# Kernel tuning notes

Hardware: AMD Instinct MI355X
Metric: run time of the kernel (lower is better)

## Reference

```python
import jax, jax.numpy as jnp
import numpy as np


def _eta(pos, conj):
    # e[0] = pos[:,1::2] repeated into even/odd cols; e[1] = (+/-)pos[:,0::2] likewise
    c = jnp.repeat(pos[:, 1::2], 2, axis=1)
    s = jnp.repeat(pos[:, 0::2], 2, axis=1)
    return jnp.stack([c, s if conj else -s])  # [2, N, d]


def setup_inputs() -> dict:
    key = jax.random.key(0)
    ks = jax.random.split(key, 8)
    B, N, d, H = 8, 4096, 128, 4
    s = 0.02
    return {
        "x": jax.random.normal(ks[0], (B, N, d), jnp.float32),
        "pos": jax.random.normal(ks[1], (N, d), jnp.float32),
        "W_lt": jax.random.normal(ks[2], (d, d), jnp.float32) * s,
        "W_phi": jax.random.normal(ks[3], (d * H, d), jnp.float32) * s,
        "b_phi": jnp.zeros((d * H,), jnp.float32),
        "W_c1": jax.random.normal(ks[4], (H, H), jnp.float32) * s,
        "b_c1": jnp.zeros((H,), jnp.float32),
        "W_c2": jax.random.normal(ks[5], (1, H), jnp.float32) * s,
        "b_c2": jnp.zeros((1,), jnp.float32),
        "ln_g": jnp.ones((d,), jnp.float32),
        "ln_b": jnp.zeros((d,), jnp.float32),
        "W_f1": jax.random.normal(ks[6], (d, d), jnp.float32) * s,
        "b_f1": jnp.zeros((d,), jnp.float32),
        "W_f2": jax.random.normal(ks[7], (d, d), jnp.float32) * s,
        "b_f2": jnp.zeros((d,), jnp.float32),
    }


def reference(x, pos, W_lt, W_phi, b_phi, W_c1, b_c1, W_c2, b_c2,
              ln_g, ln_b, W_f1, b_f1, W_f2, b_f2):
    B, N, d = x.shape
    H = W_phi.shape[0] // d
    x = x @ W_lt.T                                   # linear_trans (no bias)
    e = _eta(pos, False)                             # [2,N,d]
    xe = x[None] * e[:, None]                        # [2,B,N,d]
    # A = ones(N,N) - I  =>  A @ v == sum over nodes minus self
    f = xe.sum(axis=2, keepdims=True) - xe           # [2,B,N,d]
    f_norm = jnp.sqrt(f[0] ** 2 + f[1] ** 2)         # [B,N,d]
    phi = ((x + pos[None]) @ W_phi.T + b_phi).reshape(B, N, H, d)
    # ReLU1(|f| - phi): relu(min(1, f_norm - phi))
    res = jax.nn.relu(jnp.minimum(1.0, f_norm[:, :, None, :] - phi))  # [B,N,H,d]
    ce = _eta(pos, True)
    fec = f[0] * ce[0][None] - f[1] * ce[1][None]    # [B,N,d]
    rfe = res * fec[:, :, None, :]                   # [B,N,H,d]
    # inverse transform: (1/N) * (M @ A) with A symmetric => sum-minus-self over node dim
    inv = (rfe.sum(axis=1, keepdims=True) - rfe) / N  # [B,N,H,d]
    t = inv.transpose(0, 1, 3, 2)                    # [B,N,d,H]
    comb = (jax.nn.relu(t @ W_c1.T + b_c1) @ W_c2.T + b_c2)[..., 0]  # [B,N,d]
    m = x + comb
    mu = m.mean(-1, keepdims=True)
    var = ((m - mu) ** 2).mean(-1, keepdims=True)
    mn = (m - mu) * jax.lax.rsqrt(var + 1e-6) * ln_g + ln_b
    return jax.nn.relu(mn @ W_f1.T + b_f1) @ W_f2.T + b_f2
```

## Files before the change

kernel.cpp:

```cpp
#include <hip/hip_runtime.h>
#include <hip/hip_bf16.h>


#define DEV __device__ __forceinline__

typedef __attribute__((ext_vector_type(8))) short bf16x8;
typedef __attribute__((ext_vector_type(4))) float f32x4;

constexpr int Bb = 8, Nn = 4096;
constexpr int BN = Bb * Nn;
constexpr int LDP = 136;

union U8 { ushort u[8]; uint4 v; };

static DEV ushort f2bf(float f) {
    __hip_bfloat16 h = __float2bfloat16(f);
    return *reinterpret_cast<ushort*>(&h);
}

template <int MODE>
__global__ __launch_bounds__(256) void k_mfma_gemm(
    const float* __restrict__ X, const float* __restrict__ W,
    const float* __restrict__ bias, const float* __restrict__ pos,
    float* __restrict__ outF, ushort* __restrict__ outB,
    float* __restrict__ PS, float* __restrict__ PT,
    const float* __restrict__ S0c, const float* __restrict__ S1c)
{
    __shared__ __align__(16) ushort xs[64 * LDP];
    __shared__ __align__(16) ushort wsl[128 * LDP];
    __shared__ float red[256];
    const int t = threadIdx.x;
    const int row0 = blockIdx.x * 64;
    const int jt = (MODE == 1) ? blockIdx.y : 0;

    red[t] = 0.f;

    {
        #pragma unroll
        for (int i = 0; i < 4; ++i) {
            int e = t + i * 256, r = e >> 4, c = (e & 15) * 8;
            const float* p = X + (size_t)(row0 + r) * 128 + c;
            float4 a = *reinterpret_cast<const float4*>(p);
            float4 b = *reinterpret_cast<const float4*>(p + 4);
            if (MODE == 1) {
                int n = (row0 + r) & (Nn - 1);
                const float* q = pos + (size_t)n * 128 + c;
                float4 pa = *reinterpret_cast<const float4*>(q);
                float4 pb = *reinterpret_cast<const float4*>(q + 4);
                a.x += pa.x; a.y += pa.y; a.z += pa.z; a.w += pa.w;
                b.x += pb.x; b.y += pb.y; b.z += pb.z; b.w += pb.w;
            }
            U8 u;
            u.u[0] = f2bf(a.x); u.u[1] = f2bf(a.y); u.u[2] = f2bf(a.z); u.u[3] = f2bf(a.w);
            u.u[4] = f2bf(b.x); u.u[5] = f2bf(b.y); u.u[6] = f2bf(b.z); u.u[7] = f2bf(b.w);
            *reinterpret_cast<uint4*>(xs + r * LDP + c) = u.v;
        }
    }
    {
        const float* Wt = W + (size_t)jt * 128 * 128;
        #pragma unroll
        for (int i = 0; i < 8; ++i) {
            int e = t + i * 256, r = e >> 4, c = (e & 15) * 8;
            const float* p = Wt + (size_t)r * 128 + c;
            float4 a = *reinterpret_cast<const float4*>(p);
            float4 b = *reinterpret_cast<const float4*>(p + 4);
            U8 u;
            u.u[0] = f2bf(a.x); u.u[1] = f2bf(a.y); u.u[2] = f2bf(a.z); u.u[3] = f2bf(a.w);
            u.u[4] = f2bf(b.x); u.u[5] = f2bf(b.y); u.u[6] = f2bf(b.z); u.u[7] = f2bf(b.w);
            *reinterpret_cast<uint4*>(wsl + r * LDP + c) = u.v;
        }
    }
    __syncthreads();

    const int w = t >> 6, l = t & 63;
    const int lr = l & 15;
    const int lk = (l >> 4) * 8;

    f32x4 acc[8];
    #pragma unroll
    for (int cf = 0; cf < 8; ++cf) acc[cf] = f32x4{0.f, 0.f, 0.f, 0.f};

    #pragma unroll
    for (int ks = 0; ks < 4; ++ks) {
        bf16x8 a = *reinterpret_cast<const bf16x8*>(xs + (w * 16 + lr) * LDP + ks * 32 + lk);
        #pragma unroll
        for (int cf = 0; cf < 8; ++cf) {
            bf16x8 b = *reinterpret_cast<const bf16x8*>(wsl + (cf * 16 + lr) * LDP + ks * 32 + lk);
            acc[cf] = __builtin_amdgcn_mfma_f32_16x16x32_bf16(a, b, acc[cf], 0, 0, 0);
        }
    }

    const int bidb = row0 >> 12;
    #pragma unroll
    for (int cf = 0; cf < 8; ++cf) {
        int col = cf * 16 + lr;
        if (MODE == 0) {
            float s0c = 0.f, s1c = 0.f;
            #pragma unroll
            for (int reg = 0; reg < 4; ++reg) {
                int r = row0 + w * 16 + (l >> 4) * 4 + reg;
                float o = acc[cf][reg];
                outF[(size_t)r * 128 + col] = o;
                int n = r & (Nn - 1);
                float2 p2 = *reinterpret_cast<const float2*>(pos + (size_t)n * 128 + (col & ~1));
                s0c += o * p2.y;
                s1c += o * p2.x;
            }
            s0c += __shfl_xor(s0c, 16); s0c += __shfl_xor(s0c, 32);
            s1c += __shfl_xor(s1c, 16); s1c += __shfl_xor(s1c, 32);
            if ((l >> 4) == 0) {
                atomicAdd(&red[col], s0c);
                atomicAdd(&red[128 + col], s1c);
            }
        } else {
            float S0v = S0c[bidb * 128 + col];
            float S1v = S1c[bidb * 128 + col];
            float bv = bias[jt * 128 + col];
            float tp = 0.f;
            #pragma unroll
            for (int reg = 0; reg < 4; ++reg) {
                int r = row0 + w * 16 + (l >> 4) * 4 + reg;
                float o = acc[cf][reg] + bv;
                outB[(size_t)r * 512 + jt * 128 + col] = f2bf(o);
                int n = r & (Nn - 1);
                float xv = X[(size_t)r * 128 + col];
                float2 p2 = *reinterpret_cast<const float2*>(pos + (size_t)n * 128 + (col & ~1));
                float cc = p2.y, ss = p2.x;
                float f0 = S0v - xv * cc;
                float f1 = xv * ss - S1v;
                float fn = sqrtf(f0 * f0 + f1 * f1);
                float fec = f0 * cc - f1 * ss;
                float res = fmaxf(0.f, fminf(1.f, fn - o));
                tp += res * fec;
            }
            tp += __shfl_xor(tp, 16); tp += __shfl_xor(tp, 32);
            if ((l >> 4) == 0) atomicAdd(&red[col], tp);
        }
    }
    __syncthreads();
    if (MODE == 0) {
        PS[(size_t)blockIdx.x * 256 + t] = red[t];
    } else if (t < 128) {
        PT[((size_t)blockIdx.x * 4 + jt) * 128 + t] = red[t];
    }
}

__global__ __launch_bounds__(256) void k_finS(
    const float* __restrict__ PS, float* __restrict__ S0, float* __restrict__ S1)
{
    int b = blockIdx.x, t = threadIdx.x;
    float s = 0.f;
    #pragma unroll 8
    for (int c = 0; c < 64; ++c) s += PS[(size_t)(b * 64 + c) * 256 + t];
    if (t < 128) S0[b * 128 + t] = s;
    else         S1[b * 128 + (t - 128)] = s;
}

__global__ __launch_bounds__(256) void k_finT(
    const float* __restrict__ PT, float* __restrict__ T)
{
    int idx = blockIdx.x * 256 + threadIdx.x;
    int b = idx >> 9, lo = idx & 511;
    float s = 0.f;
    #pragma unroll 8
    for (int c = 0; c < 64; ++c) s += PT[(size_t)b * 32768 + c * 512 + lo];
    T[idx] = s;
}

__global__ __launch_bounds__(256) void k_comb_ln(
    const float* __restrict__ x1, const ushort* __restrict__ phi,
    const float* __restrict__ pos, const float* __restrict__ S0,
    const float* __restrict__ S1, const float* __restrict__ T,
    const float* __restrict__ Wc1, const float* __restrict__ bc1,
    const float* __restrict__ Wc2, const float* __restrict__ bc2,
    const float* __restrict__ lng, const float* __restrict__ lnb,
    ushort* __restrict__ mnB)
{
    int w = threadIdx.x >> 6, l = threadIdx.x & 63;
    int rrow = blockIdx.x * 4 + w;
    int b = rrow >> 12;
    int n = rrow & 4095;

    float m[2];
    #pragma unroll
    for (int q = 0; q < 2; ++q) {
        int d = l + q * 64;
        float xv = x1[(size_t)rrow * 128 + d];
        float2 p2 = *reinterpret_cast<const float2*>(pos + (size_t)n * 128 + (d & ~1));
        float cc = p2.y, ss = p2.x;
        float f0 = S0[b * 128 + d] - xv * cc;
        float f1 = xv * ss - S1[b * 128 + d];
        float fn = sqrtf(f0 * f0 + f1 * f1);
        float fec = f0 * cc - f1 * ss;
        float inv[4];
        #pragma unroll
        for (int h = 0; h < 4; ++h) {
            float ph = __bfloat162float(*reinterpret_cast<const __hip_bfloat16*>(phi + (size_t)rrow * 512 + h * 128 + d));
            float res = fmaxf(0.f, fminf(1.f, fn - ph));
            float rfe = res * fec;
            inv[h] = (T[(b * 4 + h) * 128 + d] - rfe) * (1.f / (float)Nn);
        }
        float comb = bc2[0];
        #pragma unroll
        for (int h = 0; h < 4; ++h) {
            float u = bc1[h];
            #pragma unroll
            for (int h2 = 0; h2 < 4; ++h2) u += Wc1[h * 4 + h2] * inv[h2];
            comb += fmaxf(u, 0.f) * Wc2[h];
        }
        m[q] = xv + comb;
    }

    float s = m[0] + m[1];
    #pragma unroll
    for (int off = 32; off; off >>= 1) s += __shfl_xor(s, off);
    float mu = s * (1.f / 128.f);
    float d0 = m[0] - mu, d1 = m[1] - mu;
    float v = d0 * d0 + d1 * d1;
    #pragma unroll
    for (int off = 32; off; off >>= 1) v += __shfl_xor(v, off);
    float rstd = rsqrtf(v * (1.f / 128.f) + 1e-6f);
    mnB[(size_t)rrow * 128 + l]      = f2bf(d0 * rstd * lng[l] + lnb[l]);
    mnB[(size_t)rrow * 128 + l + 64] = f2bf(d1 * rstd * lng[l + 64] + lnb[l + 64]);
}

__global__ __launch_bounds__(256) void k_ffn(
    const ushort* __restrict__ mnB, const float* __restrict__ Wf1,
    const float* __restrict__ bf1, const float* __restrict__ Wf2,
    const float* __restrict__ bf2, float* __restrict__ out)
{
    __shared__ __align__(16) ushort xs[64 * LDP];
    __shared__ __align__(16) ushort wsl[128 * LDP];
    const int t = threadIdx.x;
    const int row0 = blockIdx.x * 64;

    #pragma unroll
    for (int i = 0; i < 4; ++i) {
        int e = t + i * 256, r = e >> 4, c = (e & 15) * 8;
        uint4 v = *reinterpret_cast<const uint4*>(mnB + (size_t)(row0 + r) * 128 + c);
        *reinterpret_cast<uint4*>(xs + r * LDP + c) = v;
    }
    #pragma unroll
    for (int i = 0; i < 8; ++i) {
        int e = t + i * 256, r = e >> 4, c = (e & 15) * 8;
        const float* p = Wf1 + (size_t)r * 128 + c;
        float4 a = *reinterpret_cast<const float4*>(p);
        float4 b = *reinterpret_cast<const float4*>(p + 4);
        U8 u;
        u.u[0] = f2bf(a.x); u.u[1] = f2bf(a.y); u.u[2] = f2bf(a.z); u.u[3] = f2bf(a.w);
        u.u[4] = f2bf(b.x); u.u[5] = f2bf(b.y); u.u[6] = f2bf(b.z); u.u[7] = f2bf(b.w);
        *reinterpret_cast<uint4*>(wsl + r * LDP + c) = u.v;
    }
    __syncthreads();

    const int w = t >> 6, l = t & 63;
    const int lr = l & 15;
    const int lk = (l >> 4) * 8;

    f32x4 acc[8];
    #pragma unroll
    for (int cf = 0; cf < 8; ++cf) acc[cf] = f32x4{0.f, 0.f, 0.f, 0.f};
    #pragma unroll
    for (int ks = 0; ks < 4; ++ks) {
        bf16x8 a = *reinterpret_cast<const bf16x8*>(xs + (w * 16 + lr) * LDP + ks * 32 + lk);
        #pragma unroll
        for (int cf = 0; cf < 8; ++cf) {
            bf16x8 b = *reinterpret_cast<const bf16x8*>(wsl + (cf * 16 + lr) * LDP + ks * 32 + lk);
            acc[cf] = __builtin_amdgcn_mfma_f32_16x16x32_bf16(a, b, acc[cf], 0, 0, 0);
        }
    }

    __syncthreads();

    #pragma unroll
    for (int cf = 0; cf < 8; ++cf) {
        int col = cf * 16 + lr;
        float bv = bf1[col];
        #pragma unroll
        for (int reg = 0; reg < 4; ++reg) {
            int rl = w * 16 + (l >> 4) * 4 + reg;
            xs[rl * LDP + col] = f2bf(fmaxf(acc[cf][reg] + bv, 0.f));
        }
    }
    #pragma unroll
    for (int i = 0; i < 8; ++i) {
        int e = t + i * 256, r = e >> 4, c = (e & 15) * 8;
        const float* p = Wf2 + (size_t)r * 128 + c;
        float4 a = *reinterpret_cast<const float4*>(p);
        float4 b = *reinterpret_cast<const float4*>(p + 4);
        U8 u;
        u.u[0] = f2bf(a.x); u.u[1] = f2bf(a.y); u.u[2] = f2bf(a.z); u.u[3] = f2bf(a.w);
        u.u[4] = f2bf(b.x); u.u[5] = f2bf(b.y); u.u[6] = f2bf(b.z); u.u[7] = f2bf(b.w);
        *reinterpret_cast<uint4*>(wsl + r * LDP + c) = u.v;
    }
    __syncthreads();

    #pragma unroll
    for (int cf = 0; cf < 8; ++cf) acc[cf] = f32x4{0.f, 0.f, 0.f, 0.f};
    #pragma unroll
    for (int ks = 0; ks < 4; ++ks) {
        bf16x8 a = *reinterpret_cast<const bf16x8*>(xs + (w * 16 + lr) * LDP + ks * 32 + lk);
        #pragma unroll
        for (int cf = 0; cf < 8; ++cf) {
            bf16x8 b = *reinterpret_cast<const bf16x8*>(wsl + (cf * 16 + lr) * LDP + ks * 32 + lk);
            acc[cf] = __builtin_amdgcn_mfma_f32_16x16x32_bf16(a, b, acc[cf], 0, 0, 0);
        }
    }

    #pragma unroll
    for (int cf = 0; cf < 8; ++cf) {
        int col = cf * 16 + lr;
        float bv = bf2[col];
        #pragma unroll
        for (int reg = 0; reg < 4; ++reg) {
            int r = row0 + w * 16 + (l >> 4) * 4 + reg;
            out[(size_t)r * 128 + col] = acc[cf][reg] + bv;
        }
    }
}

extern "C" void kernel_launch(void* const* d_in, const int* in_sizes, int n_in,
                              void* d_out, int out_size, void* d_ws, size_t ws_size,
                              hipStream_t stream)
{
    const float* x    = (const float*)d_in[0];
    const float* pos  = (const float*)d_in[1];
    const float* Wlt  = (const float*)d_in[2];
    const float* Wphi = (const float*)d_in[3];
    const float* bphi = (const float*)d_in[4];
    const float* Wc1  = (const float*)d_in[5];
    const float* bc1  = (const float*)d_in[6];
    const float* Wc2  = (const float*)d_in[7];
    const float* bc2  = (const float*)d_in[8];
    const float* lng  = (const float*)d_in[9];
    const float* lnb  = (const float*)d_in[10];
    const float* Wf1  = (const float*)d_in[11];
    const float* bf1  = (const float*)d_in[12];
    const float* Wf2  = (const float*)d_in[13];
    const float* bf2  = (const float*)d_in[14];

    float* ws = (float*)d_ws;
    float* x1   = ws;
    ushort* mnB = (ushort*)(ws + 4194304);
    float* S0   = ws + 6291456;
    float* S1   = S0 + 1024;
    float* T    = S1 + 1024;
    float* PS   = T + 4096;
    float* PT   = PS + 131072;
    ushort* phi = (ushort*)(PT + 262144);
    float* out  = (float*)d_out;

    k_mfma_gemm<0><<<dim3(BN / 64), 256, 0, stream>>>(
        x, Wlt, nullptr, pos, x1, nullptr, PS, nullptr, nullptr, nullptr);
    k_finS<<<dim3(Bb), 256, 0, stream>>>(PS, S0, S1);
    k_mfma_gemm<1><<<dim3(BN / 64, 4), 256, 0, stream>>>(
        x1, Wphi, bphi, pos, nullptr, phi, nullptr, PT, S0, S1);
    k_finT<<<dim3(16), 256, 0, stream>>>(PT, T);
    k_comb_ln<<<dim3(BN / 4), 256, 0, stream>>>(x1, phi, pos, S0, S1, T,
                                                Wc1, bc1, Wc2, bc2, lng, lnb, mnB);
    k_ffn<<<dim3(BN / 64), 256, 0, stream>>>(mnB, Wf1, bf1, Wf2, bf2, out);
}
```

Baseline: 84.75 us.

## Store x1 as bf16, stage GEMM outputs through LDS, split reductions into kernels

The intermediate x1 is now stored in bf16 instead of fp32, and both GEMM epilogues write their tiles through shared memory so the global stores are coalesced 16-byte writes. The per-column S and T reductions, previously fused into the GEMM epilogues with LDS atomics, move into two new streaming reduction kernels. The aim is to cut global traffic and the strided scalar stores and atomics in the GEMMs. In exchange it adds two launches, rereads x1 and phi, and loses precision because x1 is rounded to bf16 before the later elementwise math.

Measured after the change: 71.44 us. 15.7% less time.

```diff
diff --git a/kernel.cpp b/kernel.cpp
--- a/kernel.cpp
+++ b/kernel.cpp
@@ -15,44 +15,56 @@
 
 static DEV ushort f2bf(float f) {
     __hip_bfloat16 h = __float2bfloat16(f);
-    return *reinterpret_cast<ushort*>(&h);
+    return *reinterpret_cast<unsigned short*>(&h);
+}
+static DEV float bf2f(ushort u) {
+    return __bfloat162float(*reinterpret_cast<const __hip_bfloat16*>(&u));
 }
 
 template <int MODE>
 __global__ __launch_bounds__(256) void k_mfma_gemm(
-    const float* __restrict__ X, const float* __restrict__ W,
+    const void* __restrict__ Xv, const float* __restrict__ W,
     const float* __restrict__ bias, const float* __restrict__ pos,
-    float* __restrict__ outF, ushort* __restrict__ outB,
-    float* __restrict__ PS, float* __restrict__ PT,
-    const float* __restrict__ S0c, const float* __restrict__ S1c)
+    ushort* __restrict__ outB)
 {
     __shared__ __align__(16) ushort xs[64 * LDP];
     __shared__ __align__(16) ushort wsl[128 * LDP];
-    __shared__ float red[256];
     const int t = threadIdx.x;
     const int row0 = blockIdx.x * 64;
     const int jt = (MODE == 1) ? blockIdx.y : 0;
 
-    red[t] = 0.f;
-
-    {
+    if (MODE == 0) {
+        const float* X = (const float*)Xv;
         #pragma unroll
         for (int i = 0; i < 4; ++i) {
             int e = t + i * 256, r = e >> 4, c = (e & 15) * 8;
             const float* p = X + (size_t)(row0 + r) * 128 + c;
             float4 a = *reinterpret_cast<const float4*>(p);
             float4 b = *reinterpret_cast<const float4*>(p + 4);
-            if (MODE == 1) {
-                int n = (row0 + r) & (Nn - 1);
-                const float* q = pos + (size_t)n * 128 + c;
-                float4 pa = *reinterpret_cast<const float4*>(q);
-                float4 pb = *reinterpret_cast<const float4*>(q + 4);
-                a.x += pa.x; a.y += pa.y; a.z += pa.z; a.w += pa.w;
-                b.x += pb.x; b.y += pb.y; b.z += pb.z; b.w += pb.w;
-            }
             U8 u;
             u.u[0] = f2bf(a.x); u.u[1] = f2bf(a.y); u.u[2] = f2bf(a.z); u.u[3] = f2bf(a.w);
             u.u[4] = f2bf(b.x); u.u[5] = f2bf(b.y); u.u[6] = f2bf(b.z); u.u[7] = f2bf(b.w);
+            *reinterpret_cast<uint4*>(xs + r * LDP + c) = u.v;
+        }
+    } else {
+        const ushort* X = (const ushort*)Xv;
+        #pragma unroll
+        for (int i = 0; i < 4; ++i) {
+            int e = t + i * 256, r = e >> 4, c = (e & 15) * 8;
+            U8 u;
+            u.v = *reinterpret_cast<const uint4*>(X + (size_t)(row0 + r) * 128 + c);
+            int n = (row0 + r) & (Nn - 1);
+            const float* q = pos + (size_t)n * 128 + c;
+            float4 pa = *reinterpret_cast<const float4*>(q);
+            float4 pb = *reinterpret_cast<const float4*>(q + 4);
+            u.u[0] = f2bf(bf2f(u.u[0]) + pa.x);
+            u.u[1] = f2bf(bf2f(u.u[1]) + pa.y);
+            u.u[2] = f2bf(bf2f(u.u[2]) + pa.z);
+            u.u[3] = f2bf(bf2f(u.u[3]) + pa.w);
+            u.u[4] = f2bf(bf2f(u.u[4]) + pb.x);
+            u.u[5] = f2bf(bf2f(u.u[5]) + pb.y);
+            u.u[6] = f2bf(bf2f(u.u[6]) + pb.z);
+            u.u[7] = f2bf(bf2f(u.u[7]) + pb.w);
             *reinterpret_cast<uint4*>(xs + r * LDP + c) = u.v;
         }
     }
@@ -90,59 +102,64 @@
         }
     }
 
-    const int bidb = row0 >> 12;
+    __syncthreads();
+
     #pragma unroll
     for (int cf = 0; cf < 8; ++cf) {
         int col = cf * 16 + lr;
-        if (MODE == 0) {
-            float s0c = 0.f, s1c = 0.f;
-            #pragma unroll
-            for (int reg = 0; reg < 4; ++reg) {
-                int r = row0 + w * 16 + (l >> 4) * 4 + reg;
-                float o = acc[cf][reg];
-                outF[(size_t)r * 128 + col] = o;
-                int n = r & (Nn - 1);
-                float2 p2 = *reinterpret_cast<const float2*>(pos + (size_t)n * 128 + (col & ~1));
-                s0c += o * p2.y;
-                s1c += o * p2.x;
-            }
-            s0c += __shfl_xor(s0c, 16); s0c += __shfl_xor(s0c, 32);
-            s1c += __shfl_xor(s1c, 16); s1c += __shfl_xor(s1c, 32);
-            if ((l >> 4) == 0) {
-                atomicAdd(&red[col], s0c);
-                atomicAdd(&red[128 + col], s1c);
-            }
-        } else {
-            float S0v = S0c[bidb * 128 + col];
-            float S1v = S1c[bidb * 128 + col];
-            float bv = bias[jt * 128 + col];
-            float tp = 0.f;
-            #pragma unroll
-            for (int reg = 0; reg < 4; ++reg) {
-                int r = row0 + w * 16 + (l >> 4) * 4 + reg;
-                float o = acc[cf][reg] + bv;
-                outB[(size_t)r * 512 + jt * 128 + col] = f2bf(o);
-                int n = r & (Nn - 1);
-                float xv = X[(size_t)r * 128 + col];
-                float2 p2 = *reinterpret_cast<const float2*>(pos + (size_t)n * 128 + (col & ~1));
-                float cc = p2.y, ss = p2.x;
-                float f0 = S0v - xv * cc;
-                float f1 = xv * ss - S1v;
-                float fn = sqrtf(f0 * f0 + f1 * f1);
-                float fec = f0 * cc - f1 * ss;
-                float res = fmaxf(0.f, fminf(1.f, fn - o));
-                tp += res * fec;
-            }
-            tp += __shfl_xor(tp, 16); tp += __shfl_xor(tp, 32);
-            if ((l >> 4) == 0) atomicAdd(&red[col], tp);
-        }
-    }
-    __syncthreads();
-    if (MODE == 0) {
-        PS[(size_t)blockIdx.x * 256 + t] = red[t];
-    } else if (t < 128) {
-        PT[((size_t)blockIdx.x * 4 + jt) * 128 + t] = red[t];
-    }
+        float bv = (MODE == 1) ? bias[jt * 128 + col] : 0.f;
+        #pragma unroll
+        for (int reg = 0; reg < 4; ++reg) {
+            int rl = w * 16 + (l >> 4) * 4 + reg;
+            xs[rl * LDP + col] = f2bf(acc[cf][reg] + bv);
+        }
+    }
+    __syncthreads();
+
+    #pragma unroll
+    for (int i = 0; i < 4; ++i) {
+        int e = t + i * 256, r = e >> 4, c = (e & 15) * 8;
+        uint4 v = *reinterpret_cast<const uint4*>(xs + r * LDP + c);
+        if (MODE == 0)
+            *reinterpret_cast<uint4*>(outB + (size_t)(row0 + r) * 128 + c) = v;
+        else
+            *reinterpret_cast<uint4*>(outB + (size_t)(row0 + r) * 512 + jt * 128 + c) = v;
+    }
+}
+
+__global__ __launch_bounds__(256) void k_reduceS(
+    const ushort* __restrict__ x1b, const float* __restrict__ pos,
+    float* __restrict__ PS)
+{
+    int b = blockIdx.x >> 6, c64 = blockIdx.x & 63;
+    int rr = threadIdx.x >> 5, d0 = (threadIdx.x & 31) * 4;
+    float a0[4] = {0,0,0,0}, a1[4] = {0,0,0,0};
+    #pragma unroll
+    for (int i = 0; i < 8; ++i) {
+        int n = c64 * 64 + i * 8 + rr;
+        size_t r = (size_t)b * Nn + n;
+        ushort4 xv = *reinterpret_cast<const ushort4*>(x1b + r * 128 + d0);
+        float4 p = *reinterpret_cast<const float4*>(pos + (size_t)n * 128 + d0);
+        float x0 = bf2f(xv.x), x1 = bf2f(xv.y), x2 = bf2f(xv.z), x3 = bf2f(xv.w);
+        a0[0] += x0 * p.y; a1[0] += x0 * p.x;
+        a0[1] += x1 * p.y; a1[1] += x1 * p.x;
+        a0[2] += x2 * p.w; a1[2] += x2 * p.z;
+        a0[3] += x3 * p.w; a1[3] += x3 * p.z;
+    }
+    __shared__ float redA[8][128], redB[8][128];
+    #pragma unroll
+    for (int j = 0; j < 4; ++j) { redA[rr][d0 + j] = a0[j]; redB[rr][d0 + j] = a1[j]; }
+    __syncthreads();
+    int tt = threadIdx.x;
+    float s = 0.f;
+    if (tt < 128) {
+        #pragma unroll
+        for (int k = 0; k < 8; ++k) s += redA[k][tt];
+    } else {
+        #pragma unroll
+        for (int k = 0; k < 8; ++k) s += redB[k][tt - 128];
+    }
+    PS[(size_t)blockIdx.x * 256 + tt] = s;
 }
 
 __global__ __launch_bounds__(256) void k_finS(
@@ -156,6 +173,64 @@
     else         S1[b * 128 + (t - 128)] = s;
 }
 
+__global__ __launch_bounds__(256) void k_reduceT(
+    const ushort* __restrict__ x1b, const ushort* __restrict__ phi,
+    const float* __restrict__ pos, const float* __restrict__ S0,
+    const float* __restrict__ S1, float* __restrict__ PT)
+{
+    int b = blockIdx.x >> 6, c64 = blockIdx.x & 63;
+    int rr = threadIdx.x >> 5, d0 = (threadIdx.x & 31) * 4;
+    float4 S0v = *reinterpret_cast<const float4*>(S0 + b * 128 + d0);
+    float4 S1v = *reinterpret_cast<const float4*>(S1 + b * 128 + d0);
+    float acc[4][4];
+    #pragma unroll
+    for (int h = 0; h < 4; ++h)
+        #pragma unroll
+        for (int j = 0; j < 4; ++j) acc[h][j] = 0.f;
+
+    #pragma unroll 2
+    for (int i = 0; i < 8; ++i) {
+        int n = c64 * 64 + i * 8 + rr;
+        size_t r = (size_t)b * Nn + n;
+        ushort4 xv4 = *reinterpret_cast<const ushort4*>(x1b + r * 128 + d0);
+        float4 p = *reinterpret_cast<const float4*>(pos + (size_t)n * 128 + d0);
+        float xv[4] = {bf2f(xv4.x), bf2f(xv4.y), bf2f(xv4.z), bf2f(xv4.w)};
+        float cc[4] = {p.y, p.y, p.w, p.w};
+        float ss[4] = {p.x, p.x, p.z, p.z};
+        float fec[4], fn[4];
+        #pragma unroll
+        for (int j = 0; j < 4; ++j) {
+            float f0 = ((j < 2) ? ((j == 0) ? S0v.x : S0v.y) : ((j == 2) ? S0v.z : S0v.w)) - xv[j] * cc[j];
+            float f1 = xv[j] * ss[j] - ((j < 2) ? ((j == 0) ? S1v.x : S1v.y) : ((j == 2) ? S1v.z : S1v.w));
+            fn[j] = sqrtf(f0 * f0 + f1 * f1);
+            fec[j] = f0 * cc[j] - f1 * ss[j];
+        }
+        #pragma unroll
+        for (int h = 0; h < 4; ++h) {
+            ushort4 ph4 = *reinterpret_cast<const ushort4*>(phi + r * 512 + h * 128 + d0);
+            float ph[4] = {bf2f(ph4.x), bf2f(ph4.y), bf2f(ph4.z), bf2f(ph4.w)};
+            #pragma unroll
+            for (int j = 0; j < 4; ++j)
+                acc[h][j] += fmaxf(0.f, fminf(1.f, fn[j] - ph[j])) * fec[j];
+        }
+    }
+    __shared__ float red[8][512];
+    #pragma unroll
+    for (int h = 0; h < 4; ++h)
+        #pragma unroll
+        for (int j = 0; j < 4; ++j) red[rr][h * 128 + d0 + j] = acc[h][j];
+    __syncthreads();
+    int tt = threadIdx.x;
+    #pragma unroll
+    for (int q = 0; q < 2; ++q) {
+        int idx = tt + q * 256;
+        float s = 0.f;
+        #pragma unroll
+        for (int k = 0; k < 8; ++k) s += red[k][idx];
+        PT[(size_t)blockIdx.x * 512 + idx] = s;
+    }
+}
+
 __global__ __launch_bounds__(256) void k_finT(
     const float* __restrict__ PT, float* __restrict__ T)
 {
@@ -168,7 +243,7 @@
 }
 
 __global__ __launch_bounds__(256) void k_comb_ln(
-    const float* __restrict__ x1, const ushort* __restrict__ phi,
+    const ushort* __restrict__ x1b, const ushort* __restrict__ phi,
     const float* __restrict__ pos, const float* __restrict__ S0,
     const float* __restrict__ S1, const float* __restrict__ T,
     const float* __restrict__ Wc1, const float* __restrict__ bc1,
@@ -180,25 +255,30 @@
     int rrow = blockIdx.x * 4 + w;
     int b = rrow >> 12;
     int n = rrow & 4095;
+    int d0 = 2 * l;
+    size_t r = (size_t)rrow;
+
+    ushort2 xv2 = *reinterpret_cast<const ushort2*>(x1b + r * 128 + d0);
+    float2 p2 = *reinterpret_cast<const float2*>(pos + (size_t)n * 128 + d0);
+    float2 s0 = *reinterpret_cast<const float2*>(S0 + b * 128 + d0);
+    float2 s1 = *reinterpret_cast<const float2*>(S1 + b * 128 + d0);
+    float cc = p2.y, ss = p2.x;
 
     float m[2];
+    float xv[2] = {bf2f(xv2.x), bf2f(xv2.y)};
+    float S0a[2] = {s0.x, s0.y}, S1a[2] = {s1.x, s1.y};
     #pragma unroll
     for (int q = 0; q < 2; ++q) {
-        int d = l + q * 64;
-        float xv = x1[(size_t)rrow * 128 + d];
-        float2 p2 = *reinterpret_cast<const float2*>(pos + (size_t)n * 128 + (d & ~1));
-        float cc = p2.y, ss = p2.x;
-        float f0 = S0[b * 128 + d] - xv * cc;
-        float f1 = xv * ss - S1[b * 128 + d];
+        float f0 = S0a[q] - xv[q] * cc;
+        float f1 = xv[q] * ss - S1a[q];
         float fn = sqrtf(f0 * f0 + f1 * f1);
         float fec = f0 * cc - f1 * ss;
         float inv[4];
         #pragma unroll
         for (int h = 0; h < 4; ++h) {
-            float ph = __bfloat162float(*reinterpret_cast<const __hip_bfloat16*>(phi + (size_t)rrow * 512 + h * 128 + d));
+            float ph = bf2f(phi[r * 512 + h * 128 + d0 + q]);
             float res = fmaxf(0.f, fminf(1.f, fn - ph));
-            float rfe = res * fec;
-            inv[h] = (T[(b * 4 + h) * 128 + d] - rfe) * (1.f / (float)Nn);
+            inv[h] = (T[(b * 4 + h) * 128 + d0 + q] - res * fec) * (1.f / (float)Nn);
         }
         float comb = bc2[0];
         #pragma unroll
@@ -208,20 +288,22 @@
             for (int h2 = 0; h2 < 4; ++h2) u += Wc1[h * 4 + h2] * inv[h2];
             comb += fmaxf(u, 0.f) * Wc2[h];
         }
-        m[q] = xv + comb;
+        m[q] = xv[q] + comb;
     }
 
     float s = m[0] + m[1];
     #pragma unroll
     for (int off = 32; off; off >>= 1) s += __shfl_xor(s, off);
     float mu = s * (1.f / 128.f);
-    float d0 = m[0] - mu, d1 = m[1] - mu;
-    float v = d0 * d0 + d1 * d1;
+    float e0 = m[0] - mu, e1 = m[1] - mu;
+    float v = e0 * e0 + e1 * e1;
     #pragma unroll
     for (int off = 32; off; off >>= 1) v += __shfl_xor(v, off);
     float rstd = rsqrtf(v * (1.f / 128.f) + 1e-6f);
-    mnB[(size_t)rrow * 128 + l]      = f2bf(d0 * rstd * lng[l] + lnb[l]);
-    mnB[(size_t)rrow * 128 + l + 64] = f2bf(d1 * rstd * lng[l + 64] + lnb[l + 64]);
+    ushort2 o;
+    o.x = f2bf(e0 * rstd * lng[d0] + lnb[d0]);
+    o.y = f2bf(e1 * rstd * lng[d0 + 1] + lnb[d0 + 1]);
+    *reinterpret_cast<ushort2*>(mnB + r * 128 + d0) = o;
 }
 
 __global__ __launch_bounds__(256) void k_ffn(
@@ -340,23 +422,23 @@
     const float* bf2  = (const float*)d_in[14];
 
     float* ws = (float*)d_ws;
-    float* x1   = ws;
-    ushort* mnB = (ushort*)(ws + 4194304);
-    float* S0   = ws + 6291456;
+    ushort* x1b = (ushort*)ws;
+    ushort* mnB = (ushort*)(ws + 2097152);
+    float* S0   = ws + 4194304;
     float* S1   = S0 + 1024;
     float* T    = S1 + 1024;
     float* PS   = T + 4096;
     float* PT   = PS + 131072;
-    ushort* phi = (ushort*)(PT + 262144);
+    ushort* phi = (ushort*)(ws + 4593664);
     float* out  = (float*)d_out;
 
-    k_mfma_gemm<0><<<dim3(BN / 64), 256, 0, stream>>>(
-        x, Wlt, nullptr, pos, x1, nullptr, PS, nullptr, nullptr, nullptr);
+    k_mfma_gemm<0><<<dim3(BN / 64), 256, 0, stream>>>(x, Wlt, nullptr, pos, x1b);
+    k_reduceS<<<dim3(512), 256, 0, stream>>>(x1b, pos, PS);
     k_finS<<<dim3(Bb), 256, 0, stream>>>(PS, S0, S1);
-    k_mfma_gemm<1><<<dim3(BN / 64, 4), 256, 0, stream>>>(
-        x1, Wphi, bphi, pos, nullptr, phi, nullptr, PT, S0, S1);
+    k_mfma_gemm<1><<<dim3(BN / 64, 4), 256, 0, stream>>>(x1b, Wphi, bphi, pos, phi);
+    k_reduceT<<<dim3(512), 256, 0, stream>>>(x1b, phi, pos, S0, S1, PT);
     k_finT<<<dim3(16), 256, 0, stream>>>(PT, T);
-    k_comb_ln<<<dim3(BN / 4), 256, 0, stream>>>(x1, phi, pos, S0, S1, T,
+    k_comb_ln<<<dim3(BN / 4), 256, 0, stream>>>(x1b, phi, pos, S0, S1, T,
                                                 Wc1, bc1, Wc2, bc2, lng, lnb, mnB);
     k_ffn<<<dim3(BN / 64), 256, 0, stream>>>(mnB, Wf1, bf1, Wf2, bf2, out);
 }
```
